# Kernel tuning notes

Hardware: AMD Instinct MI355X
Metric: run time of the kernel (lower is better)

## Reference

```python
import jax, jax.numpy as jnp
import numpy as np

NEG_BIG = -9e15
ALPHA = 0.2  # LeakyReLU negative slope


def setup_inputs() -> dict:
    key = jax.random.key(0)
    k1, k2, k3, k4 = jax.random.split(key, 4)
    N, F_in, F_out = 8192, 256, 64
    inp = jax.random.normal(k1, (N, F_in), dtype=jnp.float32)
    adj = jax.random.randint(k2, (N, N), 0, 2, dtype=jnp.int32)
    W = jax.random.normal(k3, (F_in, F_out), dtype=jnp.float32) * 0.05
    a = jax.random.normal(k4, (2 * F_out, 1), dtype=jnp.float32) * 0.05
    return {"input": inp, "adj": adj, "W": W, "a": a}


def reference(input, adj, W, a):
    # h = X W : [N, F_out]
    h = input @ W
    F_out = W.shape[1]
    # a_input[i,j] = concat(h_i, h_j); a_input @ a = h@a1 broadcast over j + h@a2 broadcast over i.
    a1 = a[:F_out, 0]   # [F_out]
    a2 = a[F_out:, 0]   # [F_out]
    s1 = h @ a1         # [N]
    s2 = h @ a2         # [N]
    e = jax.nn.leaky_relu(s1[:, None] + s2[None, :], negative_slope=ALPHA)  # [N, N]
    att = jnp.where(adj > 0, e, jnp.float32(NEG_BIG))
    att = jax.nn.softmax(att, axis=1)
    # dropout is identity in eval mode (training=False)
    h_prime = att @ h   # [N, F_out]
    return jax.nn.elu(h_prime)
```

## Files before the change

### kernel.cpp

```cpp
#include <hip/hip_runtime.h>
#include <hip/hip_bf16.h>

typedef __bf16 bf16_t;
typedef __attribute__((ext_vector_type(8))) __bf16 bf16x8;
typedef __attribute__((ext_vector_type(4))) __bf16 bf16x4;
typedef __attribute__((ext_vector_type(4))) float floatx4;
typedef __attribute__((ext_vector_type(4))) int intx4;

#define NN 8192
#define FIN 256
#define FOUT 64
#define GAT_ALPHA 0.2f
#define NSLICE 8
#define JS (NN / NSLICE)
#define NJB (JS / 32)
#define IB 64

typedef const __attribute__((address_space(1))) void gv_t;
typedef __attribute__((address_space(3))) void lv_t;
#define GLOAD16(gp, lp) \
    __builtin_amdgcn_global_load_lds((gv_t*)(gp), (lv_t*)(lp), 16, 0, 0)

__global__ __launch_bounds__(256) void gat_h_kernel(
    const float* __restrict__ input,
    const float* __restrict__ W,
    const float* __restrict__ a,
    bf16_t* __restrict__ hTf,
    float* __restrict__ e1g, float* __restrict__ f1g,
    float* __restrict__ e2g, float* __restrict__ f2g)
{
    alignas(16) __shared__ bf16_t in_lds[32][264];
    alignas(16) __shared__ bf16_t wt_lds[64][264];
    __shared__ float h_lds[32][65];

    const int t  = threadIdx.x;
    const int i0 = blockIdx.x * 32;

    #pragma unroll
    for (int v = 0; v < 8; v++) {
        int u  = v * 256 + t;
        int i  = u >> 6;
        int k4 = (u & 63) * 4;
        floatx4 x = *(const floatx4*)(input + (size_t)(i0 + i) * FIN + k4);
        bf16x4 b;
        #pragma unroll
        for (int e = 0; e < 4; e++) b[e] = (bf16_t)x[e];
        *(bf16x4*)(&in_lds[i][k4]) = b;
    }
    #pragma unroll
    for (int v = 0; v < 16; v++) {
        int u  = v * 256 + t;
        int k  = u >> 4;
        int f4 = (u & 15) * 4;
        floatx4 wv = *(const floatx4*)(W + k * FOUT + f4);
        #pragma unroll
        for (int e = 0; e < 4; e++) wt_lds[f4 + e][k] = (bf16_t)wv[e];
    }
    __syncthreads();

    const int wave = t >> 6;
    const int lane = t & 63;
    const int i16  = (wave & 1) * 16;
    const int f32  = (wave >> 1) * 32;
    const int lm   = lane & 15;
    const int lq   = lane >> 4;

    floatx4 acc0 = {0.f, 0.f, 0.f, 0.f};
    floatx4 acc1 = {0.f, 0.f, 0.f, 0.f};
    #pragma unroll
    for (int ks = 0; ks < 8; ks++) {
        int ko = ks * 32 + lq * 8;
        bf16x8 af = *(const bf16x8*)(&in_lds[i16 + lm][ko]);
        bf16x8 b0 = *(const bf16x8*)(&wt_lds[f32 + lm][ko]);
        bf16x8 b1 = *(const bf16x8*)(&wt_lds[f32 + 16 + lm][ko]);
        acc0 = __builtin_amdgcn_mfma_f32_16x16x32_bf16(af, b0, acc0, 0, 0, 0);
        acc1 = __builtin_amdgcn_mfma_f32_16x16x32_bf16(af, b1, acc1, 0, 0, 0);
    }

    {
        const int jb  = i0 >> 5;
        const int lqp = (i16 >> 3) + (lq >> 1);
        const int e0  = (lq & 1) * 4;
        #pragma unroll
        for (int c = 0; c < 2; c++) {
            floatx4 acc = c ? acc1 : acc0;
            int ft = (f32 >> 4) + c;
            bf16x4 hp;
            #pragma unroll
            for (int r = 0; r < 4; r++) hp[r] = (bf16_t)acc[r];
            *(bf16x4*)(hTf + (size_t)(((jb * 4 + ft) * 64 + lqp * 16 + lm) * 8 + e0)) = hp;
        }
    }
    #pragma unroll
    for (int c = 0; c < 2; c++) {
        floatx4 acc = c ? acc1 : acc0;
        #pragma unroll
        for (int r = 0; r < 4; r++)
            h_lds[i16 + lq * 4 + r][f32 + c * 16 + lm] = acc[r];
    }
    __syncthreads();

    if (t < 64) {
        int r   = t & 31;
        int sel = t >> 5;
        const float* av = a + sel * FOUT;
        float s = 0.f;
        #pragma unroll 8
        for (int f = 0; f < FOUT; f++) s += h_lds[r][f] * av[f];
        int gi = i0 + r;
        float E = expf(s);
        float F = expf(GAT_ALPHA * s);
        if (sel == 0) { e1g[gi] = E; f1g[gi] = F; }
        else          { e2g[gi] = E; f2g[gi] = F; }
    }
}

__global__ __launch_bounds__(256) void gat_pack_kernel(
    const int* __restrict__ adj,
    unsigned long long* __restrict__ bits)
{
    const int tid = blockIdx.x * 256 + threadIdx.x;
    const int r   = tid >> 7;
    const int c   = tid & 127;
    const int* src = adj + (size_t)r * NN + c * 64;
    unsigned int lo = 0, hi = 0;
    #pragma unroll
    for (int u = 0; u < 8; u++) {
        intx4 v = *(const intx4*)(src + u * 4);
        #pragma unroll
        for (int e = 0; e < 4; e++)
            lo |= (v[e] > 0 ? 1u : 0u) << (u * 4 + e);
    }
    #pragma unroll
    for (int u = 0; u < 8; u++) {
        intx4 v = *(const intx4*)(src + 32 + u * 4);
        #pragma unroll
        for (int e = 0; e < 4; e++)
            hi |= (v[e] > 0 ? 1u : 0u) << (u * 4 + e);
    }
    bits[(size_t)r * 128 + c] = ((unsigned long long)hi << 32) | lo;
}

__global__ __launch_bounds__(256, 4) void gat_att_kernel(
    const unsigned char* __restrict__ bits,
    const bf16_t* __restrict__ hTf,
    const float* __restrict__ e1g, const float* __restrict__ f1g,
    const float* __restrict__ e2g, const float* __restrict__ f2g,
    float* __restrict__ pacc,
    float* __restrict__ prs)
{
    __shared__ unsigned char bitsL[IB][128];
    __shared__ float e2l[JS], f2l[JS];

    const int t     = threadIdx.x;
    const int i0    = blockIdx.x * IB;
    const int slice = blockIdx.y;
    const int jbase = slice * JS;

    const int wave = t >> 6;
    const int lane = t & 63;
    const int lm   = lane & 15;
    const int lq   = lane >> 4;

    #pragma unroll
    for (int h = 0; h < 2; h++) {
        int r0 = wave * 16 + h * 8;
        int r  = r0 + (lane >> 3);
        int g  = (lane & 7) ^ (r & 7);
        GLOAD16(bits + (size_t)(i0 + r) * 1024 + slice * 128 + g * 16,
                &bitsL[r0][0]);
    }
    {
        int o = wave * 256;
        GLOAD16(e2g + jbase + o + lane * 4, e2l + o);
        GLOAD16(f2g + jbase + o + lane * 4, f2l + o);
    }
    __syncthreads();

    const int   row = wave * 16 + lm;
    const float E1  = e1g[i0 + row];
    const float F1  = f1g[i0 + row];

    floatx4 acc0 = {0.f,0.f,0.f,0.f}, acc1 = {0.f,0.f,0.f,0.f};
    floatx4 acc2 = {0.f,0.f,0.f,0.f}, acc3 = {0.f,0.f,0.f,0.f};
    floatx4 accR = {0.f,0.f,0.f,0.f};
    bf16x8 ones;
    #pragma unroll
    for (int e = 0; e < 8; e++) ones[e] = (bf16_t)1.0f;

    const bf16_t* hslice = hTf + (size_t)slice * NJB * 2048 + (size_t)lane * 8;

    #pragma unroll 8
    for (int jb = 0; jb < NJB; jb++) {
        int off = (((jb >> 2) ^ (row & 7)) << 4) | ((jb & 3) << 2);
        int wrd = *(const int*)(&bitsL[row][off]);
        unsigned bt = ((unsigned)wrd >> (lq * 8)) & 0xffu;

        int jo = jb * 32 + lq * 8;
        floatx4 e2a = *(const floatx4*)(&e2l[jo]);
        floatx4 e2b = *(const floatx4*)(&e2l[jo + 4]);
        floatx4 f2a = *(const floatx4*)(&f2l[jo]);
        floatx4 f2b = *(const floatx4*)(&f2l[jo + 4]);
        bf16x8 frag;
        #pragma unroll
        for (int e = 0; e < 4; e++) {
            float w0 = fmaxf(E1 * e2a[e], F1 * f2a[e]);
            frag[e]     = (bt & (1u << e))       ? (bf16_t)w0 : (bf16_t)0.f;
            float w1 = fmaxf(E1 * e2b[e], F1 * f2b[e]);
            frag[e + 4] = (bt & (1u << (e + 4))) ? (bf16_t)w1 : (bf16_t)0.f;
        }

        const bf16_t* hb = hslice + (size_t)jb * 2048;
        bf16x8 b0 = *(const bf16x8*)(hb);
        bf16x8 b1 = *(const bf16x8*)(hb + 512);
        bf16x8 b2 = *(const bf16x8*)(hb + 1024);
        bf16x8 b3 = *(const bf16x8*)(hb + 1536);
        acc0 = __builtin_amdgcn_mfma_f32_16x16x32_bf16(frag, b0, acc0, 0, 0, 0);
        acc1 = __builtin_amdgcn_mfma_f32_16x16x32_bf16(frag, b1, acc1, 0, 0, 0);
        acc2 = __builtin_amdgcn_mfma_f32_16x16x32_bf16(frag, b2, acc2, 0, 0, 0);
        acc3 = __builtin_amdgcn_mfma_f32_16x16x32_bf16(frag, b3, acc3, 0, 0, 0);
        accR = __builtin_amdgcn_mfma_f32_16x16x32_bf16(frag, ones, accR, 0, 0, 0);
    }

    if (lm == 0) {
        #pragma unroll
        for (int r = 0; r < 4; r++)
            prs[(size_t)slice * NN + i0 + wave * 16 + lq * 4 + r] = accR[r];
    }

    float* pa = pacc + (size_t)slice * NN * FOUT
                     + (size_t)(i0 + wave * 16) * FOUT;
    #pragma unroll
    for (int ft = 0; ft < 4; ft++) {
        floatx4 acc = (ft == 0) ? acc0 : (ft == 1) ? acc1
                    : (ft == 2) ? acc2 : acc3;
        #pragma unroll
        for (int r = 0; r < 4; r++)
            pa[(size_t)(lq * 4 + r) * FOUT + ft * 16 + lm] = acc[r];
    }
}

__global__ __launch_bounds__(256) void gat_combine_kernel(
    const float* __restrict__ pacc,
    const float* __restrict__ prs,
    float* __restrict__ out)
{
    int idx = blockIdx.x * 256 + threadIdx.x;
    int i   = idx >> 4;
    floatx4 s = {0.f, 0.f, 0.f, 0.f};
    float rs  = 0.f;
    #pragma unroll
    for (int p = 0; p < NSLICE; p++) {
        floatx4 v = *(const floatx4*)(pacc + (size_t)p * NN * FOUT + (size_t)idx * 4);
        s += v;
        rs += prs[p * NN + i];
    }
    float rinv = (rs > 0.f) ? 1.0f / rs : 0.f;
    floatx4 r;
    #pragma unroll
    for (int e = 0; e < 4; e++) {
        float x = s[e] * rinv;
        r[e] = (x > 0.f) ? x : (expf(x) - 1.0f);
    }
    *(floatx4*)(out + (size_t)idx * 4) = r;
}

extern "C" void kernel_launch(void* const* d_in, const int* in_sizes, int n_in,
                              void* d_out, int out_size, void* d_ws, size_t ws_size,
                              hipStream_t stream) {
    const float* input = (const float*)d_in[0];
    const int*   adj   = (const int*)d_in[1];
    const float* W     = (const float*)d_in[2];
    const float* a     = (const float*)d_in[3];
    float*       out   = (float*)d_out;

    char* ws = (char*)d_ws;
    bf16_t* hTf = (bf16_t*)ws;
    float*  e1g = (float*)(ws + (1 << 20));
    float*  f1g = e1g + NN;
    float*  e2g = f1g + NN;
    float*  f2g = e2g + NN;
    unsigned long long* bitsw = (unsigned long long*)(f2g + NN);
    float*  pacc = (float*)((char*)bitsw + NN * 128 * 8);
    float*  prs  = pacc + (size_t)NSLICE * NN * FOUT;

    gat_pack_kernel<<<NN * NN / 64 / 256, 256, 0, stream>>>(adj, bitsw);
    gat_h_kernel<<<NN / 32, 256, 0, stream>>>(input, W, a, hTf,
                                              e1g, f1g, e2g, f2g);
    dim3 gridB(NN / IB, NSLICE);
    gat_att_kernel<<<gridB, 256, 0, stream>>>((const unsigned char*)bitsw, hTf,
                                              e1g, f1g, e2g, f2g, pacc, prs);
    gat_combine_kernel<<<NN * FOUT / 4 / 256, 256, 0, stream>>>(pacc, prs, out);
}
```

Before: 406.8 us.

## Fuse adjacency bit-packing into attention kernel, dropping separate pack pass

Removes the standalone pack kernel that converted the int32 adjacency matrix into a global bitmask. Instead, each attention block reads its own 64-row by 1024-column adjacency tile directly, builds nibbles per lane, combines them with a lane shuffle into bytes, and writes them swizzled into shared memory. This saves one kernel launch plus the bitmask write and read-back through global memory. In exchange, the attention kernel's prologue now streams 256KB of int32 per block before compute starts, with less latency hiding than the earlier async LDS loads.

```diff
diff --git a/kernel.cpp b/kernel.cpp
--- a/kernel.cpp
+++ b/kernel.cpp
@@ -115,34 +115,8 @@
     }
 }
 
-__global__ __launch_bounds__(256) void gat_pack_kernel(
+__global__ __launch_bounds__(256, 4) void gat_att_kernel(
     const int* __restrict__ adj,
-    unsigned long long* __restrict__ bits)
-{
-    const int tid = blockIdx.x * 256 + threadIdx.x;
-    const int r   = tid >> 7;
-    const int c   = tid & 127;
-    const int* src = adj + (size_t)r * NN + c * 64;
-    unsigned int lo = 0, hi = 0;
-    #pragma unroll
-    for (int u = 0; u < 8; u++) {
-        intx4 v = *(const intx4*)(src + u * 4);
-        #pragma unroll
-        for (int e = 0; e < 4; e++)
-            lo |= (v[e] > 0 ? 1u : 0u) << (u * 4 + e);
-    }
-    #pragma unroll
-    for (int u = 0; u < 8; u++) {
-        intx4 v = *(const intx4*)(src + 32 + u * 4);
-        #pragma unroll
-        for (int e = 0; e < 4; e++)
-            hi |= (v[e] > 0 ? 1u : 0u) << (u * 4 + e);
-    }
-    bits[(size_t)r * 128 + c] = ((unsigned long long)hi << 32) | lo;
-}
-
-__global__ __launch_bounds__(256, 4) void gat_att_kernel(
-    const unsigned char* __restrict__ bits,
     const bf16_t* __restrict__ hTf,
     const float* __restrict__ e1g, const float* __restrict__ f1g,
     const float* __restrict__ e2g, const float* __restrict__ f2g,
@@ -162,18 +136,28 @@
     const int lm   = lane & 15;
     const int lq   = lane >> 4;
 
-    #pragma unroll
-    for (int h = 0; h < 2; h++) {
-        int r0 = wave * 16 + h * 8;
-        int r  = r0 + (lane >> 3);
-        int g  = (lane & 7) ^ (r & 7);
-        GLOAD16(bits + (size_t)(i0 + r) * 1024 + slice * 128 + g * 16,
-                &bitsL[r0][0]);
-    }
     {
         int o = wave * 256;
         GLOAD16(e2g + jbase + o + lane * 4, e2l + o);
         GLOAD16(f2g + jbase + o + lane * 4, f2l + o);
+    }
+
+    #pragma unroll 8
+    for (int k = 0; k < 64; k++) {
+        const int idx = wave * 64 + k;
+        const int r   = idx >> 2;
+        const int q   = idx & 3;
+        intx4 v = *(const intx4*)(adj + (size_t)(i0 + r) * NN
+                                      + jbase + q * 256 + lane * 4);
+        unsigned nib = (v[0] > 0 ? 1u : 0u) | (v[1] > 0 ? 2u : 0u)
+                     | (v[2] > 0 ? 4u : 0u) | (v[3] > 0 ? 8u : 0u);
+        unsigned pn  = (unsigned)__shfl_xor((int)nib, 1);
+        if (!(lane & 1)) {
+            unsigned char byte = (unsigned char)(nib | (pn << 4));
+            int bIdx = q * 32 + (lane >> 1);
+            int swz  = (((bIdx >> 4) ^ (r & 7)) << 4) | (bIdx & 15);
+            bitsL[r][swz] = byte;
+        }
     }
     __syncthreads();
 
@@ -280,15 +264,13 @@
     float*  f1g = e1g + NN;
     float*  e2g = f1g + NN;
     float*  f2g = e2g + NN;
-    unsigned long long* bitsw = (unsigned long long*)(f2g + NN);
-    float*  pacc = (float*)((char*)bitsw + NN * 128 * 8);
+    float*  pacc = f2g + NN;
     float*  prs  = pacc + (size_t)NSLICE * NN * FOUT;
 
-    gat_pack_kernel<<<NN * NN / 64 / 256, 256, 0, stream>>>(adj, bitsw);
     gat_h_kernel<<<NN / 32, 256, 0, stream>>>(input, W, a, hTf,
                                               e1g, f1g, e2g, f2g);
     dim3 gridB(NN / IB, NSLICE);
-    gat_att_kernel<<<gridB, 256, 0, stream>>>((const unsigned char*)bitsw, hTf,
+    gat_att_kernel<<<gridB, 256, 0, stream>>>(adj, hTf,
                                               e1g, f1g, e2g, f2g, pacc, prs);
     gat_combine_kernel<<<NN * FOUT / 4 / 256, 256, 0, stream>>>(pacc, prs, out);
 }
```

Measured after the change: 411.8 us. Within noise of the previous version (+1.2%).

## Pack adjacency with wave ballots and coalesced loads, permute h and e2 layouts

Applied to the files above, without the earlier changes.

The adjacency packing kernel now assigns one wave per row. Each lane reads consecutive int4 vectors, so global loads are fully coalesced, and __ballot builds the 64-bit masks in an interleaved bit order. To match that bit order, the h-transpose writes in gat_h_kernel and the e2/f2 staging into LDS in the attention kernel are permuted. The 256MB adjacency read is the dominant memory cost, and the old per-thread strided reads were poorly coalesced. The trade-off is scalar scattered bf16 stores in the h kernel, which replace vector stores.

```diff
diff --git a/kernel.cpp b/kernel.cpp
--- a/kernel.cpp
+++ b/kernel.cpp
@@ -16,10 +16,41 @@
 #define NJB (JS / 32)
 #define IB 64
 
+
 typedef const __attribute__((address_space(1))) void gv_t;
 typedef __attribute__((address_space(3))) void lv_t;
 #define GLOAD16(gp, lp) \
     __builtin_amdgcn_global_load_lds((gv_t*)(gp), (lv_t*)(lp), 16, 0, 0)
+
+__global__ __launch_bounds__(256) void gat_pack_kernel(
+    const int* __restrict__ adj,
+    unsigned long long* __restrict__ bits)
+{
+    const int wave = threadIdx.x >> 6;
+    const int lane = threadIdx.x & 63;
+    const int row  = blockIdx.x * 4 + wave;
+    const int* rp  = adj + (size_t)row * NN;
+
+    #pragma unroll
+    for (int half = 0; half < 2; half++) {
+        unsigned long long acc = 0;
+        #pragma unroll
+        for (int g2 = 0; g2 < 16; g2++) {
+            intx4 v = *(const intx4*)(rp + (half * 16 + g2) * 256 + lane * 4);
+            unsigned long long m0 = __ballot(v[0] > 0);
+            unsigned long long m1 = __ballot(v[1] > 0);
+            unsigned long long m2 = __ballot(v[2] > 0);
+            unsigned long long m3 = __ballot(v[3] > 0);
+            if ((lane >> 2) == g2) {
+                unsigned long long m = (lane & 1)
+                    ? ((lane & 2) ? m3 : m1)
+                    : ((lane & 2) ? m2 : m0);
+                acc = m;
+            }
+        }
+        bits[(size_t)row * 128 + half * 64 + lane] = acc;
+    }
+}
 
 __global__ __launch_bounds__(256) void gat_h_kernel(
     const float* __restrict__ input,
@@ -78,17 +109,21 @@
     }
 
     {
-        const int jb  = i0 >> 5;
-        const int lqp = (i16 >> 3) + (lq >> 1);
-        const int e0  = (lq & 1) * 4;
+        const int G    = i0 >> 8;
+        const int p0   = (i0 & 255) >> 2;
+        const int hi5  = p0 >> 5;
+        const int lqp  = (p0 >> 3) & 3;
+        const int enew = (i16 >> 2) + lq;
         #pragma unroll
         for (int c = 0; c < 2; c++) {
             floatx4 acc = c ? acc1 : acc0;
             int ft = (f32 >> 4) + c;
-            bf16x4 hp;
             #pragma unroll
-            for (int r = 0; r < 4; r++) hp[r] = (bf16_t)acc[r];
-            *(bf16x4*)(hTf + (size_t)(((jb * 4 + ft) * 64 + lqp * 16 + lm) * 8 + e0)) = hp;
+            for (int r = 0; r < 4; r++) {
+                int jbv = G * 8 + r * 2 + hi5;
+                size_t idx = ((size_t)(jbv * 4 + ft) * 64 + lqp * 16 + lm) * 8 + enew;
+                hTf[idx] = (bf16_t)acc[r];
+            }
         }
     }
     #pragma unroll
@@ -115,32 +150,6 @@
     }
 }
 
-__global__ __launch_bounds__(256) void gat_pack_kernel(
-    const int* __restrict__ adj,
-    unsigned long long* __restrict__ bits)
-{
-    const int tid = blockIdx.x * 256 + threadIdx.x;
-    const int r   = tid >> 7;
-    const int c   = tid & 127;
-    const int* src = adj + (size_t)r * NN + c * 64;
-    unsigned int lo = 0, hi = 0;
-    #pragma unroll
-    for (int u = 0; u < 8; u++) {
-        intx4 v = *(const intx4*)(src + u * 4);
-        #pragma unroll
-        for (int e = 0; e < 4; e++)
-            lo |= (v[e] > 0 ? 1u : 0u) << (u * 4 + e);
-    }
-    #pragma unroll
-    for (int u = 0; u < 8; u++) {
-        intx4 v = *(const intx4*)(src + 32 + u * 4);
-        #pragma unroll
-        for (int e = 0; e < 4; e++)
-            hi |= (v[e] > 0 ? 1u : 0u) << (u * 4 + e);
-    }
-    bits[(size_t)r * 128 + c] = ((unsigned long long)hi << 32) | lo;
-}
-
 __global__ __launch_bounds__(256, 4) void gat_att_kernel(
     const unsigned char* __restrict__ bits,
     const bf16_t* __restrict__ hTf,
@@ -171,9 +180,14 @@
                 &bitsL[r0][0]);
     }
     {
-        int o = wave * 256;
-        GLOAD16(e2g + jbase + o + lane * 4, e2l + o);
-        GLOAD16(f2g + jbase + o + lane * 4, f2l + o);
+        floatx4 ev = *(const floatx4*)(e2g + jbase + t * 4);
+        floatx4 fv = *(const floatx4*)(f2g + jbase + t * 4);
+        int base = (t >> 6) * 256 + (t & 63);
+        #pragma unroll
+        for (int e = 0; e < 4; e++) {
+            e2l[base + e * 64] = ev[e];
+            f2l[base + e * 64] = fv[e];
+        }
     }
     __syncthreads();
 
@@ -281,10 +295,10 @@
     float*  e2g = f1g + NN;
     float*  f2g = e2g + NN;
     unsigned long long* bitsw = (unsigned long long*)(f2g + NN);
-    float*  pacc = (float*)((char*)bitsw + NN * 128 * 8);
+    float*  pacc = (float*)((char*)bitsw + (size_t)NN * 128 * 8);
     float*  prs  = pacc + (size_t)NSLICE * NN * FOUT;
 
-    gat_pack_kernel<<<NN * NN / 64 / 256, 256, 0, stream>>>(adj, bitsw);
+    gat_pack_kernel<<<NN / 4, 256, 0, stream>>>(adj, bitsw);
     gat_h_kernel<<<NN / 32, 256, 0, stream>>>(input, W, a, hTf,
                                               e1g, f1g, e2g, f2g);
     dim3 gridB(NN / IB, NSLICE);
```

Result: no change. 400.7 us (-1.5%).
